# Kernel optimization log

Measured on AMD Instinct MI355X. Metric: run time of the kernel, lower is better.

Reference implementation:

```python
import jax, jax.numpy as jnp
import numpy as np

# Fixed rendering constants (non-tensor forward args of the module)
THETA_RANGE = (0.0, float(np.pi) / 2.0)
PHI_RANGE = (-float(np.pi) / 2.0, float(np.pi) / 2.0)
R_RANGE = (0.5, 2.5)
C_LIGHT = 1.0          # speed of light (normalized units)
DELTA_T = 0.03125      # time-bin width -> step = C_LIGHT*DELTA_T = (2.0/64)
SCALING_MODIFIER = 1.0
USE_OCCLUSION = True
SH_C0 = 0.28209479177387814
G = 2048


def quat_to_rotmat(q):
    # q: [G,4] (w,x,y,z), unnormalized -> [G,3,3]
    q = q / (jnp.linalg.norm(q, axis=-1, keepdims=True) + 1e-12)
    w, x, y, z = q[:, 0], q[:, 1], q[:, 2], q[:, 3]
    R = jnp.stack([
        1 - 2 * (y * y + z * z), 2 * (x * y - w * z), 2 * (x * z + w * y),
        2 * (x * y + w * z), 1 - 2 * (x * x + z * z), 2 * (y * z - w * x),
        2 * (x * z - w * y), 2 * (y * z + w * x), 1 - 2 * (x * x + y * y),
    ], axis=-1)
    return R.reshape(-1, 3, 3)


def setup_inputs() -> dict:
    key = jax.random.key(0)
    k1, k2, k3, k4, k5 = jax.random.split(key, 5)
    # Gaussians clustered in front of the sensor (camera at origin, +z hemisphere)
    gaussian_means = jax.random.normal(k1, (G, 3), jnp.float32) * 0.5 + jnp.array([0.0, 0.0, 1.5], jnp.float32)
    gaussian_scales = jax.random.normal(k2, (G, 3), jnp.float32) * 0.3 - 2.5   # log-scales -> exp ~ 0.08
    gaussian_rotations = jax.random.normal(k3, (G, 4), jnp.float32)
    gaussian_opacities = jax.random.normal(k4, (G, 1), jnp.float32)
    gaussian_features = jax.random.normal(k5, (G, 3), jnp.float32) * 0.5
    camera_pos = jnp.zeros((3,), jnp.float32)
    return {
        "gaussian_means": gaussian_means,
        "gaussian_scales": gaussian_scales,
        "gaussian_rotations": gaussian_rotations,
        "gaussian_opacities": gaussian_opacities,
        "gaussian_features": gaussian_features,
        "camera_pos": camera_pos,
        "num_theta": 32,
        "num_phi": 32,
        "num_r": 64,
    }


def reference(gaussian_means, gaussian_scales, gaussian_rotations,
              gaussian_opacities, gaussian_features, camera_pos,
              num_theta, num_phi, num_r):
    # --- ray construction (module wrapper) ---
    theta = jnp.linspace(THETA_RANGE[0], THETA_RANGE[1], num_theta)
    phi = jnp.linspace(PHI_RANGE[0], PHI_RANGE[1], num_phi)
    tg, pg = jnp.meshgrid(theta, phi, indexing='ij')           # [nt,np]
    th, ph = tg.reshape(-1), pg.reshape(-1)                    # [R]
    dirs = jnp.stack([jnp.sin(th) * jnp.cos(ph),
                      jnp.sin(th) * jnp.sin(ph),
                      jnp.cos(th)], axis=1)                    # [R,3]
    t = jnp.linspace(R_RANGE[0], R_RANGE[1], num_r)            # [S]

    # --- Gaussian parameter activation ---
    scales = jnp.exp(gaussian_scales) * SCALING_MODIFIER       # [G,3]
    Rm = quat_to_rotmat(gaussian_rotations)                    # [G,3,3]
    inv_s2 = 1.0 / (scales * scales)                           # [G,3]
    prec = jnp.einsum('gij,gj,gkj->gik', Rm, inv_s2, Rm)       # Sigma^{-1} [G,3,3]
    opac = jax.nn.sigmoid(gaussian_opacities[:, 0])            # [G]
    albedo = jnp.mean(jnp.clip(SH_C0 * gaussian_features + 0.5, 0.0, None), axis=-1)  # [G]

    # --- per-(sample,ray,gaussian) Mahalanobis quadratic, factored in t ---
    # (o + t d - mu)^T P (o + t d - mu) = A[r,g] t^2 + B[r,g] t + Cq[g]
    om = camera_pos[None, :] - gaussian_means                  # [G,3]
    A = jnp.einsum('rd,gde,re->rg', dirs, prec, dirs)          # [R,G]
    B = 2.0 * jnp.einsum('rd,gde,ge->rg', dirs, prec, om)      # [R,G]
    Cq = jnp.einsum('gd,gde,ge->g', om, prec, om)              # [G]
    t2 = t * t
    quad = (A[None] * t2[:, None, None]
            + B[None] * t[:, None, None]
            + Cq[None, None])                                  # [S,R,G]
    w = opac[None, None, :] * jnp.exp(-0.5 * quad)             # [S,R,G]
    density = jnp.sum(w, axis=-1)                              # [S,R]
    rho = jnp.sum(w * albedo[None, None, :], axis=-1)          # [S,R]

    # --- sequential transmittance accumulation along the ray ---
    step = C_LIGHT * DELTA_T
    acc = jnp.cumsum(density * step, axis=0)
    acc_excl = jnp.concatenate([jnp.zeros_like(acc[:1]), acc[:-1]], axis=0)
    transmittance = jnp.exp(-acc_excl)                         # [S,R]
    rho_density = rho * transmittance if USE_OCCLUSION else rho

    # --- module post-processing ---
    result = rho_density.reshape(num_r, num_theta, num_phi)
    result = result / (t[:, None, None] ** 2 + 1e-8) * jnp.sin(tg)[None]
    dtheta = (THETA_RANGE[1] - THETA_RANGE[0]) / num_theta
    dphi = (PHI_RANGE[1] - PHI_RANGE[0]) / num_phi
    pred_histogram = jnp.sum(result, axis=(1, 2)) * dtheta * dphi
    return result, pred_histogram
```

## Files before the change

kernel.cpp:

```cpp
#include <hip/hip_runtime.h>
#include <math.h>

#define G_N   2048
#define NT    32
#define NP    32
#define NR    64
#define NRAY  (NT * NP)

__global__ __launch_bounds__(256) void k_pre(
    const float* __restrict__ means, const float* __restrict__ scales,
    const float* __restrict__ rots, const float* __restrict__ opacs,
    const float* __restrict__ feats, const float* __restrict__ cam,
    float* __restrict__ ws) {
  int g = blockIdx.x * 256 + threadIdx.x;
  if (g >= G_N) return;

  float mx = means[3*g+0], my = means[3*g+1], mz = means[3*g+2];
  float i0 = expf(-2.0f * scales[3*g+0]);
  float i1 = expf(-2.0f * scales[3*g+1]);
  float i2 = expf(-2.0f * scales[3*g+2]);

  float qw = rots[4*g+0], qx = rots[4*g+1], qy = rots[4*g+2], qz = rots[4*g+3];
  float inv = 1.0f / (sqrtf(qw*qw + qx*qx + qy*qy + qz*qz) + 1e-12f);
  qw *= inv; qx *= inv; qy *= inv; qz *= inv;

  float R00 = 1.f - 2.f*(qy*qy + qz*qz), R01 = 2.f*(qx*qy - qw*qz), R02 = 2.f*(qx*qz + qw*qy);
  float R10 = 2.f*(qx*qy + qw*qz), R11 = 1.f - 2.f*(qx*qx + qz*qz), R12 = 2.f*(qy*qz - qw*qx);
  float R20 = 2.f*(qx*qz - qw*qy), R21 = 2.f*(qy*qz + qw*qx), R22 = 1.f - 2.f*(qx*qx + qy*qy);

  float p00 = R00*R00*i0 + R01*R01*i1 + R02*R02*i2;
  float p11 = R10*R10*i0 + R11*R11*i1 + R12*R12*i2;
  float p22 = R20*R20*i0 + R21*R21*i1 + R22*R22*i2;
  float p01 = R00*R10*i0 + R01*R11*i1 + R02*R12*i2;
  float p02 = R00*R20*i0 + R01*R21*i1 + R02*R22*i2;
  float p12 = R10*R20*i0 + R11*R21*i1 + R12*R22*i2;

  float ox = cam[0] - mx, oy = cam[1] - my, oz = cam[2] - mz;
  float Px = p00*ox + p01*oy + p02*oz;
  float Py = p01*ox + p11*oy + p12*oz;
  float Pz = p02*ox + p12*oy + p22*oz;
  float Cq = ox*Px + oy*Py + oz*Pz;

  float op = 1.0f / (1.0f + expf(-opacs[g]));

  const float SH_C0 = 0.28209479177387814f;
  float a0 = fmaxf(SH_C0*feats[3*g+0] + 0.5f, 0.f);
  float a1 = fmaxf(SH_C0*feats[3*g+1] + 0.5f, 0.f);
  float a2 = fmaxf(SH_C0*feats[3*g+2] + 0.5f, 0.f);
  float alb = (a0 + a1 + a2) * (1.0f/3.0f);

  const float c = -0.7213475204444817f;
  float* o = ws + 12*g;
  o[0] = c*p00; o[1] = c*p11; o[2] = c*p22;
  o[3] = c*p01; o[4] = c*p02; o[5] = c*p12;
  o[6] = 2.f*c*Px; o[7] = 2.f*c*Py; o[8] = 2.f*c*Pz;
  o[9] = c*Cq + log2f(op);
  o[10] = alb; o[11] = 0.f;
}

__global__ __launch_bounds__(256) void k_main(const float* __restrict__ ws,
                                              float* __restrict__ out) {
  __shared__ float4 abce[G_N];
  __shared__ float red[2][4][64];

  const int ray = blockIdx.x;
  const int ti = ray >> 5;
  const int pj = ray & 31;
  const float th = (float)ti * (float)(M_PI / 2.0 / (NT - 1));
  const float ph = (float)(-M_PI / 2.0) + (float)pj * (float)(M_PI / (NP - 1));
  float sth, cth, sph, cph;
  sincosf(th, &sth, &cth);
  sincosf(ph, &sph, &cph);
  const float dx = sth * cph, dy = sth * sph, dz = cth;
  const float dxx = dx*dx, dyy = dy*dy, dzz = dz*dz;
  const float dxy = 2.f*dx*dy, dxz = 2.f*dx*dz, dyz = 2.f*dy*dz;

  const int tid = threadIdx.x;

  #pragma unroll
  for (int i = 0; i < G_N / 256; ++i) {
    int g = tid + i * 256;
    const float4* w4 = (const float4*)(ws + 12 * g);
    float4 a = w4[0], b = w4[1], cc = w4[2];
    float A2 = a.x*dxx + a.y*dyy + a.z*dzz + a.w*dxy + b.x*dxz + b.y*dyz;
    float B2 = b.z*dx + b.w*dy + cc.x*dz;
    abce[g] = make_float4(A2, B2, cc.y, cc.z);
  }
  __syncthreads();

  const int lane = tid & 63;
  const int wv = tid >> 6;
  const float t = 0.5f + (float)lane * (2.0f / 63.0f);

  const float4* base = abce + wv * (G_N / 4);
  float d0 = 0.f, d1 = 0.f, d2 = 0.f, d3 = 0.f;
  float h0 = 0.f, h1 = 0.f, h2 = 0.f, h3 = 0.f;
  #pragma unroll 4
  for (int g = 0; g < G_N / 4; g += 4) {
    float4 e0 = base[g+0];
    float4 e1 = base[g+1];
    float4 e2 = base[g+2];
    float4 e3 = base[g+3];
    float x0 = __builtin_amdgcn_exp2f(fmaf(fmaf(e0.x, t, e0.y), t, e0.z));
    float x1 = __builtin_amdgcn_exp2f(fmaf(fmaf(e1.x, t, e1.y), t, e1.z));
    float x2 = __builtin_amdgcn_exp2f(fmaf(fmaf(e2.x, t, e2.y), t, e2.z));
    float x3 = __builtin_amdgcn_exp2f(fmaf(fmaf(e3.x, t, e3.y), t, e3.z));
    d0 += x0; h0 = fmaf(x0, e0.w, h0);
    d1 += x1; h1 = fmaf(x1, e1.w, h1);
    d2 += x2; h2 = fmaf(x2, e2.w, h2);
    d3 += x3; h3 = fmaf(x3, e3.w, h3);
  }
  red[0][wv][lane] = (d0 + d1) + (d2 + d3);
  red[1][wv][lane] = (h0 + h1) + (h2 + h3);
  __syncthreads();

  if (tid < 64) {
    float D  = (red[0][0][tid] + red[0][1][tid]) + (red[0][2][tid] + red[0][3][tid]);
    float Rh = (red[1][0][tid] + red[1][1][tid]) + (red[1][2][tid] + red[1][3][tid]);
    const float step = 1.0f * 0.03125f;
    float s = D * step;
    float inc = s;
    #pragma unroll
    for (int off = 1; off < 64; off <<= 1) {
      float v = __shfl_up(inc, off, 64);
      if (tid >= off) inc += v;
    }
    float excl = inc - s;
    float T = expf(-excl);
    float tt = 0.5f + (float)tid * (2.0f / 63.0f);
    float res = Rh * T / (tt * tt + 1e-8f) * sth;
    out[tid * NRAY + ray] = res;
  }
}

__global__ __launch_bounds__(256) void k_hist(const float* __restrict__ res,
                                              float* __restrict__ hist) {
  const int t = blockIdx.x;
  const int tid = threadIdx.x;
  float s = 0.f;
  #pragma unroll
  for (int r = tid; r < NRAY; r += 256) s += res[t * NRAY + r];
  #pragma unroll
  for (int off = 32; off > 0; off >>= 1) s += __shfl_down(s, off, 64);
  __shared__ float sm[4];
  if ((tid & 63) == 0) sm[tid >> 6] = s;
  __syncthreads();
  if (tid == 0) {
    const float dtdp = (float)((M_PI / 2.0 / NT) * (M_PI / NP));
    hist[t] = ((sm[0] + sm[1]) + (sm[2] + sm[3])) * dtdp;
  }
}

extern "C" void kernel_launch(void* const* d_in, const int* in_sizes, int n_in,
                              void* d_out, int out_size, void* d_ws, size_t ws_size,
                              hipStream_t stream) {
  const float* means  = (const float*)d_in[0];
  const float* scales = (const float*)d_in[1];
  const float* rots   = (const float*)d_in[2];
  const float* opacs  = (const float*)d_in[3];
  const float* feats  = (const float*)d_in[4];
  const float* cam    = (const float*)d_in[5];

  float* ws  = (float*)d_ws;
  float* out = (float*)d_out;

  k_pre <<<G_N / 256, 256, 0, stream>>>(means, scales, rots, opacs, feats, cam, ws);
  k_main<<<NRAY,      256, 0, stream>>>(ws, out);
  k_hist<<<NR,        256, 0, stream>>>(out, out + NR * NRAY);
}
```

Baseline: 98.38 us.

## Fuse Gaussian preprocessing into main kernel and use packed FMA for quadratic evaluation

Drops the separate preprocessing kernel. Every ray block now recomputes the per-Gaussian coefficients (covariance, quadratic terms, log-opacity, albedo) straight from the raw inputs, and stores them pair-interleaved in shared memory. The inner loop evaluates two Gaussians per instruction with v_pk_fma_f32, and several expf/logf/sqrt calls become hardware exp2/log/rsq intrinsics. This saves one kernel launch and the workspace round trip, but each of the 1024 blocks now redoes the full 2048-Gaussian preprocessing, and the 1e-12 epsilon in the quaternion normalisation is dropped.

Result: no change. 97.75 us (-0.6%).

```diff
diff --git a/kernel.cpp b/kernel.cpp
--- a/kernel.cpp
+++ b/kernel.cpp
@@ -6,22 +6,30 @@
 #define NP    32
 #define NR    64
 #define NRAY  (NT * NP)
+#define NPAIR (G_N / 2)
 
-__global__ __launch_bounds__(256) void k_pre(
+typedef float f32x2 __attribute__((ext_vector_type(2)));
+
+__device__ __forceinline__ f32x2 pk_fma(f32x2 a, f32x2 b, f32x2 c) {
+  f32x2 d;
+  asm("v_pk_fma_f32 %0, %1, %2, %3" : "=v"(d) : "v"(a), "v"(b), "v"(c));
+  return d;
+}
+
+__device__ __forceinline__ float4 gauss_coef(
+    int g,
     const float* __restrict__ means, const float* __restrict__ scales,
     const float* __restrict__ rots, const float* __restrict__ opacs,
-    const float* __restrict__ feats, const float* __restrict__ cam,
-    float* __restrict__ ws) {
-  int g = blockIdx.x * 256 + threadIdx.x;
-  if (g >= G_N) return;
-
-  float mx = means[3*g+0], my = means[3*g+1], mz = means[3*g+2];
-  float i0 = expf(-2.0f * scales[3*g+0]);
-  float i1 = expf(-2.0f * scales[3*g+1]);
-  float i2 = expf(-2.0f * scales[3*g+2]);
+    const float* __restrict__ feats, float cx, float cy, float cz,
+    float dxx, float dyy, float dzz, float dxy, float dxz, float dyz,
+    float dx, float dy, float dz) {
+  const float n2log2e = -2.8853900817779268f;
+  float i0 = __builtin_amdgcn_exp2f(n2log2e * scales[3*g+0]);
+  float i1 = __builtin_amdgcn_exp2f(n2log2e * scales[3*g+1]);
+  float i2 = __builtin_amdgcn_exp2f(n2log2e * scales[3*g+2]);
 
   float qw = rots[4*g+0], qx = rots[4*g+1], qy = rots[4*g+2], qz = rots[4*g+3];
-  float inv = 1.0f / (sqrtf(qw*qw + qx*qx + qy*qy + qz*qz) + 1e-12f);
+  float inv = __builtin_amdgcn_rsqf(qw*qw + qx*qx + qy*qy + qz*qz);
   qw *= inv; qx *= inv; qy *= inv; qz *= inv;
 
   float R00 = 1.f - 2.f*(qy*qy + qz*qz), R01 = 2.f*(qx*qy - qw*qz), R02 = 2.f*(qx*qz + qw*qy);
@@ -35,13 +43,14 @@
   float p02 = R00*R20*i0 + R01*R21*i1 + R02*R22*i2;
   float p12 = R10*R20*i0 + R11*R21*i1 + R12*R22*i2;
 
-  float ox = cam[0] - mx, oy = cam[1] - my, oz = cam[2] - mz;
+  float ox = cx - means[3*g+0], oy = cy - means[3*g+1], oz = cz - means[3*g+2];
   float Px = p00*ox + p01*oy + p02*oz;
   float Py = p01*ox + p11*oy + p12*oz;
   float Pz = p02*ox + p12*oy + p22*oz;
   float Cq = ox*Px + oy*Py + oz*Pz;
 
-  float op = 1.0f / (1.0f + expf(-opacs[g]));
+  float u = __builtin_amdgcn_exp2f(-1.4426950408889634f * opacs[g]);
+  float l2op = -__builtin_amdgcn_logf(1.0f + u);
 
   const float SH_C0 = 0.28209479177387814f;
   float a0 = fmaxf(SH_C0*feats[3*g+0] + 0.5f, 0.f);
@@ -50,17 +59,19 @@
   float alb = (a0 + a1 + a2) * (1.0f/3.0f);
 
   const float c = -0.7213475204444817f;
-  float* o = ws + 12*g;
-  o[0] = c*p00; o[1] = c*p11; o[2] = c*p22;
-  o[3] = c*p01; o[4] = c*p02; o[5] = c*p12;
-  o[6] = 2.f*c*Px; o[7] = 2.f*c*Py; o[8] = 2.f*c*Pz;
-  o[9] = c*Cq + log2f(op);
-  o[10] = alb; o[11] = 0.f;
+  float A2 = c * (p00*dxx + p11*dyy + p22*dzz + p01*dxy + p02*dxz + p12*dyz);
+  float B2 = 2.f * c * (Px*dx + Py*dy + Pz*dz);
+  float Cf = c * Cq + l2op;
+  return make_float4(A2, B2, Cf, alb);
 }
 
-__global__ __launch_bounds__(256) void k_main(const float* __restrict__ ws,
-                                              float* __restrict__ out) {
-  __shared__ float4 abce[G_N];
+__global__ __launch_bounds__(256, 4) void k_main(
+    const float* __restrict__ means, const float* __restrict__ scales,
+    const float* __restrict__ rots, const float* __restrict__ opacs,
+    const float* __restrict__ feats, const float* __restrict__ cam,
+    float* __restrict__ out) {
+  __shared__ float4 ab[NPAIR];
+  __shared__ float4 ca[NPAIR];
   __shared__ float red[2][4][64];
 
   const int ray = blockIdx.x;
@@ -76,42 +87,46 @@
   const float dxy = 2.f*dx*dy, dxz = 2.f*dx*dz, dyz = 2.f*dy*dz;
 
   const int tid = threadIdx.x;
+  const float cx = cam[0], cy = cam[1], cz = cam[2];
 
   #pragma unroll
-  for (int i = 0; i < G_N / 256; ++i) {
-    int g = tid + i * 256;
-    const float4* w4 = (const float4*)(ws + 12 * g);
-    float4 a = w4[0], b = w4[1], cc = w4[2];
-    float A2 = a.x*dxx + a.y*dyy + a.z*dzz + a.w*dxy + b.x*dxz + b.y*dyz;
-    float B2 = b.z*dx + b.w*dy + cc.x*dz;
-    abce[g] = make_float4(A2, B2, cc.y, cc.z);
+  for (int i = 0; i < 4; ++i) {
+    int p = tid + i * 256;
+    float4 r0 = gauss_coef(2*p,   means, scales, rots, opacs, feats,
+                           cx, cy, cz, dxx, dyy, dzz, dxy, dxz, dyz, dx, dy, dz);
+    float4 r1 = gauss_coef(2*p+1, means, scales, rots, opacs, feats,
+                           cx, cy, cz, dxx, dyy, dzz, dxy, dxz, dyz, dx, dy, dz);
+    ab[p] = make_float4(r0.x, r1.x, r0.y, r1.y);
+    ca[p] = make_float4(r0.z, r1.z, r0.w, r1.w);
   }
   __syncthreads();
 
   const int lane = tid & 63;
   const int wv = tid >> 6;
   const float t = 0.5f + (float)lane * (2.0f / 63.0f);
+  const f32x2 tt = {t, t};
+  const f32x2 one = {1.f, 1.f};
 
-  const float4* base = abce + wv * (G_N / 4);
-  float d0 = 0.f, d1 = 0.f, d2 = 0.f, d3 = 0.f;
-  float h0 = 0.f, h1 = 0.f, h2 = 0.f, h3 = 0.f;
+  const float4* pab = ab + wv * (NPAIR / 4);
+  const float4* pca = ca + wv * (NPAIR / 4);
+  f32x2 dA = {0.f, 0.f}, dB = {0.f, 0.f};
+  f32x2 hA = {0.f, 0.f}, hB = {0.f, 0.f};
   #pragma unroll 4
-  for (int g = 0; g < G_N / 4; g += 4) {
-    float4 e0 = base[g+0];
-    float4 e1 = base[g+1];
-    float4 e2 = base[g+2];
-    float4 e3 = base[g+3];
-    float x0 = __builtin_amdgcn_exp2f(fmaf(fmaf(e0.x, t, e0.y), t, e0.z));
-    float x1 = __builtin_amdgcn_exp2f(fmaf(fmaf(e1.x, t, e1.y), t, e1.z));
-    float x2 = __builtin_amdgcn_exp2f(fmaf(fmaf(e2.x, t, e2.y), t, e2.z));
-    float x3 = __builtin_amdgcn_exp2f(fmaf(fmaf(e3.x, t, e3.y), t, e3.z));
-    d0 += x0; h0 = fmaf(x0, e0.w, h0);
-    d1 += x1; h1 = fmaf(x1, e1.w, h1);
-    d2 += x2; h2 = fmaf(x2, e2.w, h2);
-    d3 += x3; h3 = fmaf(x3, e3.w, h3);
+  for (int j = 0; j < NPAIR / 4; j += 2) {
+    float4 u0 = pab[j],     v0 = pca[j];
+    float4 u1 = pab[j + 1], v1 = pca[j + 1];
+    f32x2 A0 = {u0.x, u0.y}, B0 = {u0.z, u0.w}, C0 = {v0.x, v0.y}, L0 = {v0.z, v0.w};
+    f32x2 A1 = {u1.x, u1.y}, B1 = {u1.z, u1.w}, C1 = {v1.x, v1.y}, L1 = {v1.z, v1.w};
+    f32x2 q0 = pk_fma(pk_fma(A0, tt, B0), tt, C0);
+    f32x2 q1 = pk_fma(pk_fma(A1, tt, B1), tt, C1);
+    f32x2 x0, x1;
+    x0.x = __builtin_amdgcn_exp2f(q0.x); x0.y = __builtin_amdgcn_exp2f(q0.y);
+    x1.x = __builtin_amdgcn_exp2f(q1.x); x1.y = __builtin_amdgcn_exp2f(q1.y);
+    dA = pk_fma(x0, one, dA); hA = pk_fma(x0, L0, hA);
+    dB = pk_fma(x1, one, dB); hB = pk_fma(x1, L1, hB);
   }
-  red[0][wv][lane] = (d0 + d1) + (d2 + d3);
-  red[1][wv][lane] = (h0 + h1) + (h2 + h3);
+  red[0][wv][lane] = (dA.x + dA.y) + (dB.x + dB.y);
+  red[1][wv][lane] = (hA.x + hA.y) + (hB.x + hB.y);
   __syncthreads();
 
   if (tid < 64) {
@@ -126,9 +141,9 @@
       if (tid >= off) inc += v;
     }
     float excl = inc - s;
-    float T = expf(-excl);
-    float tt = 0.5f + (float)tid * (2.0f / 63.0f);
-    float res = Rh * T / (tt * tt + 1e-8f) * sth;
+    float T = __builtin_amdgcn_exp2f(-1.4426950408889634f * excl);
+    float tt2 = 0.5f + (float)tid * (2.0f / 63.0f);
+    float res = Rh * T / (tt2 * tt2 + 1e-8f) * sth;
     out[tid * NRAY + ray] = res;
   }
 }
@@ -161,10 +176,8 @@
   const float* feats  = (const float*)d_in[4];
   const float* cam    = (const float*)d_in[5];
 
-  float* ws  = (float*)d_ws;
   float* out = (float*)d_out;
 
-  k_pre <<<G_N / 256, 256, 0, stream>>>(means, scales, rots, opacs, feats, cam, ws);
-  k_main<<<NRAY,      256, 0, stream>>>(ws, out);
-  k_hist<<<NR,        256, 0, stream>>>(out, out + NR * NRAY);
+  k_main<<<NRAY, 256, 0, stream>>>(means, scales, rots, opacs, feats, cam, out);
+  k_hist<<<NR,   256, 0, stream>>>(out, out + NR * NRAY);
 }
```

## Fuse per-Gaussian precompute into main kernel and process four rays per block

Applied to the files above, without the earlier changes.

Drops the separate precompute kernel: each block now recomputes per-Gaussian covariance, opacity and albedo from the raw inputs and builds coefficients for four rays in shared memory. The main loop has each thread evaluate four time bins for one ray, so each shared-memory load feeds four exp2 evaluations instead of one. The block count falls to a quarter and shared memory grows to about 128KB, which limits occupancy, and the redundant per-Gaussian precompute is now repeated by every block. Transcendentals switch to hardware exp2/log/rsq intrinsics, and the 1e-12 epsilon is dropped from the quaternion normalization.

After: 99.29 us. No clear change (+0.9%).

```diff
diff --git a/kernel.cpp b/kernel.cpp
--- a/kernel.cpp
+++ b/kernel.cpp
@@ -6,130 +6,145 @@
 #define NP    32
 #define NR    64
 #define NRAY  (NT * NP)
+#define PLANE 8196
 
-__global__ __launch_bounds__(256) void k_pre(
+__global__ __launch_bounds__(256) void k_main(
     const float* __restrict__ means, const float* __restrict__ scales,
     const float* __restrict__ rots, const float* __restrict__ opacs,
     const float* __restrict__ feats, const float* __restrict__ cam,
-    float* __restrict__ ws) {
-  int g = blockIdx.x * 256 + threadIdx.x;
-  if (g >= G_N) return;
+    float* __restrict__ out) {
+  __shared__ float coef[4 * PLANE];
+  __shared__ float red[2][4][256];
 
-  float mx = means[3*g+0], my = means[3*g+1], mz = means[3*g+2];
-  float i0 = expf(-2.0f * scales[3*g+0]);
-  float i1 = expf(-2.0f * scales[3*g+1]);
-  float i2 = expf(-2.0f * scales[3*g+2]);
+  const int tid  = threadIdx.x;
+  const int ray0 = blockIdx.x * 4;
+  const int ti   = ray0 >> 5;
+  const int pj0  = ray0 & 31;
 
-  float qw = rots[4*g+0], qx = rots[4*g+1], qy = rots[4*g+2], qz = rots[4*g+3];
-  float inv = 1.0f / (sqrtf(qw*qw + qx*qx + qy*qy + qz*qz) + 1e-12f);
-  qw *= inv; qx *= inv; qy *= inv; qz *= inv;
+  const float dth = (float)(M_PI / 2.0 / (NT - 1));
+  const float dph = (float)(M_PI / (NP - 1));
+  float sth, cth;
+  sincosf((float)ti * dth, &sth, &cth);
+  const float dz = cth, dzz = dz * dz;
 
-  float R00 = 1.f - 2.f*(qy*qy + qz*qz), R01 = 2.f*(qx*qy - qw*qz), R02 = 2.f*(qx*qz + qw*qy);
-  float R10 = 2.f*(qx*qy + qw*qz), R11 = 1.f - 2.f*(qx*qx + qz*qz), R12 = 2.f*(qy*qz - qw*qx);
-  float R20 = 2.f*(qx*qz - qw*qy), R21 = 2.f*(qy*qz + qw*qx), R22 = 1.f - 2.f*(qx*qx + qy*qy);
+  float dX[4], dY[4], dXX[4], dYY[4], dXY[4], dXZ[4], dYZ[4];
+  #pragma unroll
+  for (int r = 0; r < 4; ++r) {
+    float ph = (float)(-M_PI / 2.0) + (float)(pj0 + r) * dph;
+    float sp, cp;
+    sincosf(ph, &sp, &cp);
+    float dx = sth * cp, dy = sth * sp;
+    dX[r] = dx; dY[r] = dy;
+    dXX[r] = dx * dx; dYY[r] = dy * dy;
+    dXY[r] = 2.f * dx * dy; dXZ[r] = 2.f * dx * dz; dYZ[r] = 2.f * dy * dz;
+  }
 
-  float p00 = R00*R00*i0 + R01*R01*i1 + R02*R02*i2;
-  float p11 = R10*R10*i0 + R11*R11*i1 + R12*R12*i2;
-  float p22 = R20*R20*i0 + R21*R21*i1 + R22*R22*i2;
-  float p01 = R00*R10*i0 + R01*R11*i1 + R02*R12*i2;
-  float p02 = R00*R20*i0 + R01*R21*i1 + R02*R22*i2;
-  float p12 = R10*R20*i0 + R11*R21*i1 + R12*R22*i2;
-
-  float ox = cam[0] - mx, oy = cam[1] - my, oz = cam[2] - mz;
-  float Px = p00*ox + p01*oy + p02*oz;
-  float Py = p01*ox + p11*oy + p12*oz;
-  float Pz = p02*ox + p12*oy + p22*oz;
-  float Cq = ox*Px + oy*Py + oz*Pz;
-
-  float op = 1.0f / (1.0f + expf(-opacs[g]));
-
-  const float SH_C0 = 0.28209479177387814f;
-  float a0 = fmaxf(SH_C0*feats[3*g+0] + 0.5f, 0.f);
-  float a1 = fmaxf(SH_C0*feats[3*g+1] + 0.5f, 0.f);
-  float a2 = fmaxf(SH_C0*feats[3*g+2] + 0.5f, 0.f);
-  float alb = (a0 + a1 + a2) * (1.0f/3.0f);
-
-  const float c = -0.7213475204444817f;
-  float* o = ws + 12*g;
-  o[0] = c*p00; o[1] = c*p11; o[2] = c*p22;
-  o[3] = c*p01; o[4] = c*p02; o[5] = c*p12;
-  o[6] = 2.f*c*Px; o[7] = 2.f*c*Py; o[8] = 2.f*c*Pz;
-  o[9] = c*Cq + log2f(op);
-  o[10] = alb; o[11] = 0.f;
-}
-
-__global__ __launch_bounds__(256) void k_main(const float* __restrict__ ws,
-                                              float* __restrict__ out) {
-  __shared__ float4 abce[G_N];
-  __shared__ float red[2][4][64];
-
-  const int ray = blockIdx.x;
-  const int ti = ray >> 5;
-  const int pj = ray & 31;
-  const float th = (float)ti * (float)(M_PI / 2.0 / (NT - 1));
-  const float ph = (float)(-M_PI / 2.0) + (float)pj * (float)(M_PI / (NP - 1));
-  float sth, cth, sph, cph;
-  sincosf(th, &sth, &cth);
-  sincosf(ph, &sph, &cph);
-  const float dx = sth * cph, dy = sth * sph, dz = cth;
-  const float dxx = dx*dx, dyy = dy*dy, dzz = dz*dz;
-  const float dxy = 2.f*dx*dy, dxz = 2.f*dx*dz, dyz = 2.f*dy*dz;
-
-  const int tid = threadIdx.x;
+  const float cx = cam[0], cy = cam[1], cz = cam[2];
+  const float c      = -0.7213475204444817f;
+  const float l2e    = 1.4426950408889634f;
+  const float n2l2e  = -2.8853900817779268f;
+  const float SH_C0  = 0.28209479177387814f;
 
   #pragma unroll
   for (int i = 0; i < G_N / 256; ++i) {
     int g = tid + i * 256;
-    const float4* w4 = (const float4*)(ws + 12 * g);
-    float4 a = w4[0], b = w4[1], cc = w4[2];
-    float A2 = a.x*dxx + a.y*dyy + a.z*dzz + a.w*dxy + b.x*dxz + b.y*dyz;
-    float B2 = b.z*dx + b.w*dy + cc.x*dz;
-    abce[g] = make_float4(A2, B2, cc.y, cc.z);
+    float i0 = __builtin_amdgcn_exp2f(n2l2e * scales[3*g+0]);
+    float i1 = __builtin_amdgcn_exp2f(n2l2e * scales[3*g+1]);
+    float i2 = __builtin_amdgcn_exp2f(n2l2e * scales[3*g+2]);
+
+    float qw = rots[4*g+0], qx = rots[4*g+1], qy = rots[4*g+2], qz = rots[4*g+3];
+    float inv = __builtin_amdgcn_rsqf(qw*qw + qx*qx + qy*qy + qz*qz);
+    qw *= inv; qx *= inv; qy *= inv; qz *= inv;
+
+    float R00 = 1.f - 2.f*(qy*qy + qz*qz), R01 = 2.f*(qx*qy - qw*qz), R02 = 2.f*(qx*qz + qw*qy);
+    float R10 = 2.f*(qx*qy + qw*qz), R11 = 1.f - 2.f*(qx*qx + qz*qz), R12 = 2.f*(qy*qz - qw*qx);
+    float R20 = 2.f*(qx*qz - qw*qy), R21 = 2.f*(qy*qz + qw*qx), R22 = 1.f - 2.f*(qx*qx + qy*qy);
+
+    float p00 = c*(R00*R00*i0 + R01*R01*i1 + R02*R02*i2);
+    float p11 = c*(R10*R10*i0 + R11*R11*i1 + R12*R12*i2);
+    float p22 = c*(R20*R20*i0 + R21*R21*i1 + R22*R22*i2);
+    float p01 = c*(R00*R10*i0 + R01*R11*i1 + R02*R12*i2);
+    float p02 = c*(R00*R20*i0 + R01*R21*i1 + R02*R22*i2);
+    float p12 = c*(R10*R20*i0 + R11*R21*i1 + R12*R22*i2);
+
+    float ox = cx - means[3*g+0], oy = cy - means[3*g+1], oz = cz - means[3*g+2];
+    float Px = p00*ox + p01*oy + p02*oz;
+    float Py = p01*ox + p11*oy + p12*oz;
+    float Pz = p02*ox + p12*oy + p22*oz;
+    float Cq = ox*Px + oy*Py + oz*Pz;
+
+    float u = __builtin_amdgcn_exp2f(-l2e * opacs[g]);
+    float Cf = Cq - __builtin_amdgcn_logf(1.0f + u);
+
+    float a0 = fmaxf(SH_C0*feats[3*g+0] + 0.5f, 0.f);
+    float a1 = fmaxf(SH_C0*feats[3*g+1] + 0.5f, 0.f);
+    float a2 = fmaxf(SH_C0*feats[3*g+2] + 0.5f, 0.f);
+    float alb = (a0 + a1 + a2) * (1.0f/3.0f);
+
+    #pragma unroll
+    for (int r = 0; r < 4; ++r) {
+      float A = p00*dXX[r] + p11*dYY[r] + p22*dzz + p01*dXY[r] + p02*dXZ[r] + p12*dYZ[r];
+      float B = 2.f * (Px*dX[r] + Py*dY[r] + Pz*dz);
+      *(float4*)&coef[r * PLANE + g * 4] = make_float4(A, B, Cf, alb);
+    }
   }
   __syncthreads();
 
   const int lane = tid & 63;
-  const int wv = tid >> 6;
-  const float t = 0.5f + (float)lane * (2.0f / 63.0f);
+  const int wv   = tid >> 6;
+  const int r    = lane >> 4;
+  const int tt   = lane & 15;
+  const float tstep = 2.0f / 63.0f;
+  const float t0 = 0.5f + (float)tt * tstep;
+  const float t1 = t0 + 16.f * tstep;
+  const float t2 = t0 + 32.f * tstep;
+  const float t3 = t0 + 48.f * tstep;
 
-  const float4* base = abce + wv * (G_N / 4);
+  const float4* basep = (const float4*)&coef[r * PLANE] + wv * (G_N / 4);
   float d0 = 0.f, d1 = 0.f, d2 = 0.f, d3 = 0.f;
   float h0 = 0.f, h1 = 0.f, h2 = 0.f, h3 = 0.f;
-  #pragma unroll 4
-  for (int g = 0; g < G_N / 4; g += 4) {
-    float4 e0 = base[g+0];
-    float4 e1 = base[g+1];
-    float4 e2 = base[g+2];
-    float4 e3 = base[g+3];
-    float x0 = __builtin_amdgcn_exp2f(fmaf(fmaf(e0.x, t, e0.y), t, e0.z));
-    float x1 = __builtin_amdgcn_exp2f(fmaf(fmaf(e1.x, t, e1.y), t, e1.z));
-    float x2 = __builtin_amdgcn_exp2f(fmaf(fmaf(e2.x, t, e2.y), t, e2.z));
-    float x3 = __builtin_amdgcn_exp2f(fmaf(fmaf(e3.x, t, e3.y), t, e3.z));
-    d0 += x0; h0 = fmaf(x0, e0.w, h0);
-    d1 += x1; h1 = fmaf(x1, e1.w, h1);
-    d2 += x2; h2 = fmaf(x2, e2.w, h2);
-    d3 += x3; h3 = fmaf(x3, e3.w, h3);
+  #pragma unroll 8
+  for (int g = 0; g < G_N / 4; ++g) {
+    float4 e = basep[g];
+    float q0 = fmaf(fmaf(e.x, t0, e.y), t0, e.z);
+    float q1 = fmaf(fmaf(e.x, t1, e.y), t1, e.z);
+    float q2 = fmaf(fmaf(e.x, t2, e.y), t2, e.z);
+    float q3 = fmaf(fmaf(e.x, t3, e.y), t3, e.z);
+    float x0 = __builtin_amdgcn_exp2f(q0);
+    float x1 = __builtin_amdgcn_exp2f(q1);
+    float x2 = __builtin_amdgcn_exp2f(q2);
+    float x3 = __builtin_amdgcn_exp2f(q3);
+    d0 += x0; h0 = fmaf(x0, e.w, h0);
+    d1 += x1; h1 = fmaf(x1, e.w, h1);
+    d2 += x2; h2 = fmaf(x2, e.w, h2);
+    d3 += x3; h3 = fmaf(x3, e.w, h3);
   }
-  red[0][wv][lane] = (d0 + d1) + (d2 + d3);
-  red[1][wv][lane] = (h0 + h1) + (h2 + h3);
+
+  red[0][wv][r*64 + tt     ] = d0;  red[1][wv][r*64 + tt     ] = h0;
+  red[0][wv][r*64 + tt + 16] = d1;  red[1][wv][r*64 + tt + 16] = h1;
+  red[0][wv][r*64 + tt + 32] = d2;  red[1][wv][r*64 + tt + 32] = h2;
+  red[0][wv][r*64 + tt + 48] = d3;  red[1][wv][r*64 + tt + 48] = h3;
   __syncthreads();
 
-  if (tid < 64) {
-    float D  = (red[0][0][tid] + red[0][1][tid]) + (red[0][2][tid] + red[0][3][tid]);
-    float Rh = (red[1][0][tid] + red[1][1][tid]) + (red[1][2][tid] + red[1][3][tid]);
+  {
+    const int rr = tid >> 6;
+    const int t  = tid & 63;
+    int idx = rr * 64 + t;
+    float D  = (red[0][0][idx] + red[0][1][idx]) + (red[0][2][idx] + red[0][3][idx]);
+    float Rh = (red[1][0][idx] + red[1][1][idx]) + (red[1][2][idx] + red[1][3][idx]);
     const float step = 1.0f * 0.03125f;
     float s = D * step;
     float inc = s;
     #pragma unroll
     for (int off = 1; off < 64; off <<= 1) {
       float v = __shfl_up(inc, off, 64);
-      if (tid >= off) inc += v;
+      if (t >= off) inc += v;
     }
     float excl = inc - s;
-    float T = expf(-excl);
-    float tt = 0.5f + (float)tid * (2.0f / 63.0f);
-    float res = Rh * T / (tt * tt + 1e-8f) * sth;
-    out[tid * NRAY + ray] = res;
+    float T = __builtin_amdgcn_exp2f(-1.4426950408889634f * excl);
+    float tv = 0.5f + (float)t * tstep;
+    float res = Rh * T / (tv * tv + 1e-8f) * sth;
+    out[t * NRAY + ray0 + rr] = res;
   }
 }
 
@@ -139,7 +154,7 @@
   const int tid = threadIdx.x;
   float s = 0.f;
   #pragma unroll
-  for (int r = tid; r < NRAY; r += 256) s += res[t * NRAY + r];
+  for (int rr = tid; rr < NRAY; rr += 256) s += res[t * NRAY + rr];
   #pragma unroll
   for (int off = 32; off > 0; off >>= 1) s += __shfl_down(s, off, 64);
   __shared__ float sm[4];
@@ -161,10 +176,8 @@
   const float* feats  = (const float*)d_in[4];
   const float* cam    = (const float*)d_in[5];
 
-  float* ws  = (float*)d_ws;
   float* out = (float*)d_out;
 
-  k_pre <<<G_N / 256, 256, 0, stream>>>(means, scales, rots, opacs, feats, cam, ws);
-  k_main<<<NRAY,      256, 0, stream>>>(ws, out);
-  k_hist<<<NR,        256, 0, stream>>>(out, out + NR * NRAY);
+  k_main<<<NRAY / 4, 256, 0, stream>>>(means, scales, rots, opacs, feats, cam, out);
+  k_hist<<<NR,       256, 0, stream>>>(out, out + NR * NRAY);
 }
```
